# Optimization experiments

Hardware: AMD Instinct MI355X
Metric: run time of the kernel (lower is better)

The kernel has to match this reference:

```python
import jax, jax.numpy as jnp
import numpy as np
import math

N, S, D, BF, K, NT, NL = 4096, 64, 256, 24, 8, 64, 4096

def setup_inputs() -> dict:
    key = jax.random.key(0)
    ks = jax.random.split(key, 20)
    inp = {
        "values": jax.random.normal(ks[0], (N, S), dtype=jnp.float32),
        "kinds": jax.random.randint(ks[1], (N, S), 0, K, dtype=jnp.int32),
        "mask": jax.random.randint(ks[2], (N, S), 0, 2, dtype=jnp.int32),
        "prim_type": jax.random.randint(ks[3], (N,), 0, NT, dtype=jnp.int32),
        "layer_id": jax.random.randint(ks[4], (N,), 0, NL, dtype=jnp.int32),
        "meta": jax.random.normal(ks[5], (N, 4), dtype=jnp.float32),
        # frozen Fourier projection (sigma=8)
        "B_ff": jax.random.normal(ks[6], (1, BF), dtype=jnp.float32) * 8.0,
        # embeddings (N(0,1) like nn.Embedding default)
        "kind_emb_w": jax.random.normal(ks[7], (K, D), dtype=jnp.float32),
        "type_emb_w": jax.random.normal(ks[8], (NT, D), dtype=jnp.float32),
        "layer_emb_w": jax.random.normal(ks[9], (NL, D), dtype=jnp.float32),
        # per-kind MLPs: 2B -> D -> D
        "mlp_w1": jax.random.normal(ks[10], (K, 2 * BF, D), dtype=jnp.float32) / np.sqrt(2 * BF),
        "mlp_b1": jnp.zeros((K, D), dtype=jnp.float32),
        "mlp_w2": jax.random.normal(ks[11], (K, D, D), dtype=jnp.float32) / np.sqrt(D),
        "mlp_b2": jnp.zeros((K, D), dtype=jnp.float32),
        # fuse: 3D -> D -> D
        "fuse_w1": jax.random.normal(ks[12], (3 * D, D), dtype=jnp.float32) / np.sqrt(3 * D),
        "fuse_b1": jnp.zeros((D,), dtype=jnp.float32),
        "fuse_w2": jax.random.normal(ks[13], (D, D), dtype=jnp.float32) / np.sqrt(D),
        "fuse_b2": jnp.zeros((D,), dtype=jnp.float32),
        # meta_lin: 4 -> D
        "meta_w": jax.random.normal(ks[14], (4, D), dtype=jnp.float32) / 2.0,
        "meta_b": jnp.zeros((D,), dtype=jnp.float32),
    }
    return inp

def _gelu(x):
    return jax.nn.gelu(x, approximate=False)  # torch nn.GELU default = exact erf

def reference(values, kinds, mask, prim_type, layer_id, meta, B_ff,
              kind_emb_w, type_emb_w, layer_emb_w,
              mlp_w1, mlp_b1, mlp_w2, mlp_b2,
              fuse_w1, fuse_b1, fuse_w2, fuse_b2, meta_w, meta_b):
    n, s = values.shape
    d = kind_emb_w.shape[1]
    k_kinds = kind_emb_w.shape[0]
    # Fourier features over all N*S scalar slots -> [NS, 2B]
    y = (2.0 * math.pi) * values.reshape(-1, 1) @ B_ff
    ff = jnp.concatenate([jnp.sin(y), jnp.cos(y)], axis=-1)
    kf = kinds.reshape(-1)
    # kind-routed per-kind MLP (dispatch/combine expressed as masked combine)
    out = jnp.zeros((n * s, d), dtype=values.dtype)
    for k in range(k_kinds):
        h = _gelu(ff @ mlp_w1[k] + mlp_b1[k]) @ mlp_w2[k] + mlp_b2[k]
        out = jnp.where((kf == k)[:, None], h, out)
    h_slots = out.reshape(n, s, d) + kind_emb_w[kinds]
    m = mask.astype(values.dtype)
    h_slots = h_slots * m[..., None]
    denom = jnp.clip(m.sum(axis=1, keepdims=True), 1.0)  # [N,1]
    h_num = h_slots.sum(axis=1) / denom  # masked mean pooling -> [N,D]
    h = jnp.concatenate([h_num, type_emb_w[prim_type], layer_emb_w[layer_id]], axis=-1)
    fused = _gelu(h @ fuse_w1 + fuse_b1) @ fuse_w2 + fuse_b2
    return fused + meta @ meta_w + meta_b
```

## Files before the change

kernel.cpp:

```cpp
#include <hip/hip_runtime.h>
#include <math.h>


#define WIN   256
#define ROWS  4
#define NWIN  1024

#define W2F_HI   0
#define W2F_LO   524288
#define W1F_HI   1048576
#define W1F_LO   1179648
#define FW1F_HI  1310720
#define FW1F_LO  1507328
#define FW2F_HI  1703936
#define FW2F_LO  1769472
#define POOL_BYTE 3670016ull
#define CNT_BYTE  37224448ull
#define DEN_BYTE  37355520ull

typedef __attribute__((ext_vector_type(8))) short frag;
typedef __attribute__((ext_vector_type(4))) float f32x4;

__device__ __forceinline__ unsigned short f2bf_rn(float x) {
    unsigned int u = __float_as_uint(x);
    unsigned int r = (u + 0x7fffu + ((u >> 16) & 1u)) >> 16;
    return (unsigned short)r;
}
__device__ __forceinline__ float bf2f(unsigned short h) {
    return __uint_as_float(((unsigned int)h) << 16);
}
__device__ __forceinline__ void split_bf(float x, unsigned short& h, unsigned short& l) {
    unsigned short hh = f2bf_rn(x);
    h = hh;
    l = f2bf_rn(x - bf2f(hh));
}

__device__ __forceinline__ float gelu_fast(float x) {
    float u = fabsf(x) * 0.7071067811865476f;
    float t = __builtin_amdgcn_rcpf(fmaf(0.3275911f, u, 1.0f));
    float p = fmaf(fmaf(fmaf(fmaf(1.061405429f, t, -1.453152027f), t,
                             1.421413741f), t, -0.284496736f), t, 0.254829592f) * t;
    float e = __expf(-u * u);
    float er = fmaf(-p, e, 1.0f);
    er = copysignf(er, x);
    return 0.5f * x * (1.0f + er);
}

__global__ __launch_bounds__(512) void prep_kernel(
    const float* __restrict__ w1, const float* __restrict__ w2,
    const float* __restrict__ fw1, const float* __restrict__ fw2,
    short* __restrict__ ws)
{
    int tid = blockIdx.x * 512 + threadIdx.x;
    int fid = tid >> 6, ln = tid & 63;
    if (fid >= 1792) return;
    int lr = ln & 15, kq = ln >> 4;
    float v[8];
    int dhi, dlo, dsto;
    if (fid < 1024) {
        int k = fid >> 7, kst = (fid >> 4) & 7, nt = fid & 15;
        int col = nt * 16 + lr;
        #pragma unroll
        for (int b = 0; b < 8; ++b) {
            int kg = kst * 32 + kq * 8 + b;
            v[b] = w2[(k * 256 + kg) * 256 + col];
        }
        dsto = fid * 512 + ln * 8; dhi = W2F_HI; dlo = W2F_LO;
    } else if (fid < 1280) {
        int f = fid - 1024;
        int k = f >> 5, kst = (f >> 4) & 1, nt = f & 15;
        int col = nt * 16 + lr;
        #pragma unroll
        for (int b = 0; b < 8; ++b) {
            int kg = kst * 32 + kq * 8 + b;
            v[b] = (kg < 48) ? w1[(k * 48 + kg) * 256 + col] : 0.0f;
        }
        dsto = f * 512 + ln * 8; dhi = W1F_HI; dlo = W1F_LO;
    } else if (fid < 1664) {
        int f = fid - 1280;
        int kst = f >> 4, nt = f & 15;
        int col = nt * 16 + lr;
        #pragma unroll
        for (int b = 0; b < 8; ++b) {
            int kg = kst * 32 + kq * 8 + b;
            v[b] = fw1[kg * 256 + col];
        }
        dsto = f * 512 + ln * 8; dhi = FW1F_HI; dlo = FW1F_LO;
    } else {
        int f = fid - 1664;
        int kst = f >> 4, nt = f & 15;
        int col = nt * 16 + lr;
        #pragma unroll
        for (int b = 0; b < 8; ++b) {
            int kg = kst * 32 + kq * 8 + b;
            v[b] = fw2[kg * 256 + col];
        }
        dsto = f * 512 + ln * 8; dhi = FW2F_HI; dlo = FW2F_LO;
    }
    union { unsigned short u[8]; frag f; } hu, lu;
    #pragma unroll
    for (int b = 0; b < 8; ++b) split_bf(v[b], hu.u[b], lu.u[b]);
    *(frag*)(ws + dhi + dsto) = hu.f;
    *(frag*)(ws + dlo + dsto) = lu.f;
}

__global__ __launch_bounds__(512, 4) void window_kernel(
    const float* __restrict__ values, const int* __restrict__ kinds,
    const int* __restrict__ mask, const float* __restrict__ B_ff,
    const float* __restrict__ b1, const short* __restrict__ wsf,
    float* __restrict__ poolf, float* __restrict__ cntf,
    float* __restrict__ denf)
{
    __shared__ float vals[WIN];
    __shared__ unsigned char knd[WIN], msk[WIN];
    __shared__ unsigned short list[WIN + 128];
    __shared__ short chunk_kind[32];
    __shared__ short chunk_base[32];
    __shared__ int nchT_s;
    __shared__ float Bs[24];
    __shared__ float pool_s[32 * 257];
    __shared__ __align__(16) short Asl[8][2][1024];

    const short* w1f_hi = wsf + W1F_HI;
    const short* w1f_lo = wsf + W1F_LO;

    const int t = threadIdx.x, w = blockIdx.x, base = w * WIN;
    const int wv = t >> 6, ln = t & 63, lr16 = ln & 15, kq = ln >> 4;

    for (int i = t; i < WIN; i += 512) {
        vals[i] = values[base + i];
        knd[i]  = (unsigned char)kinds[base + i];
        msk[i]  = (unsigned char)mask[base + i];
    }
    if (t < 24) Bs[t] = B_ff[t];
    __syncthreads();

    if (t < 64) {
        int cnts[8];
        #pragma unroll
        for (int k = 0; k < 8; ++k) cnts[k] = 0;
        for (int c = 0; c < WIN / 64; ++c) {
            int p = c * 64 + t;
            int kd = knd[p], mk = msk[p];
            #pragma unroll
            for (int k = 0; k < 8; ++k) {
                unsigned long long bal = __ballot(mk && (kd == k));
                cnts[k] += __popcll(bal);
            }
        }
        int offk[8], run = 0;
        #pragma unroll
        for (int k = 0; k < 8; ++k) { offk[k] = run; run += (cnts[k] + 15) & ~15; }
        int fillk[8];
        #pragma unroll
        for (int k = 0; k < 8; ++k) fillk[k] = 0;
        const unsigned long long below = (1ull << t) - 1ull;
        for (int c = 0; c < WIN / 64; ++c) {
            int p = c * 64 + t;
            int kd = knd[p], mk = msk[p];
            #pragma unroll
            for (int k = 0; k < 8; ++k) {
                unsigned long long bal = __ballot(mk && (kd == k));
                if (mk && (kd == k)) {
                    int rank = __popcll(bal & below);
                    list[offk[k] + fillk[k] + rank] = (unsigned short)p;
                }
                fillk[k] += __popcll(bal);
            }
        }
        #pragma unroll
        for (int k = 0; k < 8; ++k) {
            int padded = (cnts[k] + 15) & ~15;
            for (int i = cnts[k] + t; i < padded; i += 64) list[offk[k] + i] = 0xFFFFu;
        }
        if (t == 0) {
            int ci = 0;
            #pragma unroll
            for (int k = 0; k < 8; ++k) {
                int nk = (cnts[k] + 15) >> 4;
                for (int j = 0; j < nk; ++j) {
                    chunk_kind[ci] = (short)k;
                    chunk_base[ci] = (short)(offk[k] + j * 16);
                    ++ci;
                }
            }
            nchT_s = ci;
        }
    } else if (t < 96) {
        int i = t - 64, r = i >> 3, k = i & 7, c = 0;
        for (int s = 0; s < 64; ++s) c += (msk[r * 64 + s] && knd[r * 64 + s] == k) ? 1 : 0;
        cntf[(w * ROWS + r) * 8 + k] = (float)c;
    } else if (t < 100) {
        int r = t - 96, c = 0;
        for (int s = 0; s < 64; ++s) c += msk[r * 64 + s];
        denf[w * ROWS + r] = 1.0f / (float)(c > 0 ? c : 1);
    } else if (t >= 128) {
        for (int i = t - 128; i < 32 * 257; i += 384) pool_s[i] = 0.0f;
    }
    __syncthreads();

    const int nchT = nchT_s;

    for (int ci = wv; ci < nchT; ci += 8) {
        const int k = (int)chunk_kind[ci];
        const int cb = (int)chunk_base[ci];

        #pragma unroll
        for (int half = 0; half < 2; ++half) {
            int tt = ln + half * 64;
            int s = tt >> 3, g = tt & 7;
            union { unsigned short u[8]; frag f; } hu, lu;
            if (g < 6) {
                int e = list[cb + s];
                float v = vals[e & (WIN - 1)];
                int iscos = (g >= 3);
                int j0 = (iscos ? (g - 3) : g) * 8;
                #pragma unroll
                for (int b = 0; b < 8; ++b) {
                    float rev = __builtin_amdgcn_fractf(v * Bs[j0 + b]);
                    float sv = iscos ? __builtin_amdgcn_cosf(rev)
                                     : __builtin_amdgcn_sinf(rev);
                    split_bf(sv, hu.u[b], lu.u[b]);
                }
            } else {
                #pragma unroll
                for (int b = 0; b < 8; ++b) { hu.u[b] = 0; lu.u[b] = 0; }
            }
            int ao = s * 64 + ((g ^ (s & 7)) << 3);
            *(frag*)&Asl[wv][0][ao] = hu.f;
            *(frag*)&Asl[wv][1][ao] = lu.f;
        }
        frag ah[2], al[2];
        #pragma unroll
        for (int kst = 0; kst < 2; ++kst) {
            int gi = kst * 4 + kq;
            int ao = lr16 * 64 + ((gi ^ (lr16 & 7)) << 3);
            ah[kst] = *(const frag*)&Asl[wv][0][ao];
            al[kst] = *(const frag*)&Asl[wv][1][ao];
        }
        for (int ntg = 0; ntg < 4; ++ntg) {
            f32x4 acc[4];
            #pragma unroll
            for (int q = 0; q < 4; ++q) acc[q] = (f32x4)0.0f;
            #pragma unroll
            for (int q = 0; q < 4; ++q) {
                int nt = ntg * 4 + q;
                size_t bo0 = (((size_t)k * 2 + 0) * 16 + nt) * 512 + ln * 8;
                size_t bo1 = (((size_t)k * 2 + 1) * 16 + nt) * 512 + ln * 8;
                frag bh0 = *(const frag*)(w1f_hi + bo0);
                frag bl0 = *(const frag*)(w1f_lo + bo0);
                frag bh1 = *(const frag*)(w1f_hi + bo1);
                frag bl1 = *(const frag*)(w1f_lo + bo1);
                acc[q] = __builtin_amdgcn_mfma_f32_16x16x32_bf16(ah[0], bh0, acc[q], 0, 0, 0);
                acc[q] = __builtin_amdgcn_mfma_f32_16x16x32_bf16(al[0], bh0, acc[q], 0, 0, 0);
                acc[q] = __builtin_amdgcn_mfma_f32_16x16x32_bf16(ah[0], bl0, acc[q], 0, 0, 0);
                acc[q] = __builtin_amdgcn_mfma_f32_16x16x32_bf16(ah[1], bh1, acc[q], 0, 0, 0);
                acc[q] = __builtin_amdgcn_mfma_f32_16x16x32_bf16(al[1], bh1, acc[q], 0, 0, 0);
                acc[q] = __builtin_amdgcn_mfma_f32_16x16x32_bf16(ah[1], bl1, acc[q], 0, 0, 0);
            }
            #pragma unroll
            for (int q = 0; q < 4; ++q) {
                int nt = ntg * 4 + q;
                int col = nt * 16 + lr16;
                float b1v = b1[k * 256 + col];
                #pragma unroll
                for (int r = 0; r < 4; ++r) {
                    int s = kq * 4 + r;
                    int e = list[cb + s];
                    if (e != 0xFFFF) {
                        float g = gelu_fast(acc[q][r] + b1v);
                        atomicAdd(&pool_s[((e >> 6) * 8 + k) * 257 + col], g);
                    }
                }
            }
        }
    }
    __syncthreads();

    for (int i = t; i < 32 * 256; i += 512) {
        int rk = i >> 8, c = i & 255;
        int r = rk >> 3, k = rk & 7;
        poolf[((size_t)k * 4096 + w * ROWS + r) * 256 + c] = pool_s[rk * 257 + c];
    }
}

__global__ __launch_bounds__(512) void fuse_kernel(
    const short* __restrict__ ws, const float* __restrict__ poolf,
    const float* __restrict__ cntf, const float* __restrict__ denf,
    const int* __restrict__ pt, const int* __restrict__ lid,
    const float* __restrict__ meta, const float* __restrict__ type_emb,
    const float* __restrict__ layer_emb, const float* __restrict__ b2,
    const float* __restrict__ kind_emb, const float* __restrict__ fb1,
    const float* __restrict__ fb2, const float* __restrict__ meta_w,
    const float* __restrict__ meta_b, float* __restrict__ out)
{
    __shared__ __align__(16) short Af[2][2][4096];
    __shared__ __align__(16) float hz[4096];
    __shared__ float cnt_s[128], den_s[16], meta_s[64];
    __shared__ int pt_s[16], lid_s[16];

    const short* w2f_hi  = ws + W2F_HI;
    const short* w2f_lo  = ws + W2F_LO;
    const short* fw1f_hi = ws + FW1F_HI;
    const short* fw1f_lo = ws + FW1F_LO;
    const short* fw2f_hi = ws + FW2F_HI;
    const short* fw2f_lo = ws + FW2F_LO;

    const int t = threadIdx.x, blk = blockIdx.x, rb = blk * 16;
    const int wv = t >> 6, ln = t & 63, lr16 = ln & 15, kq = ln >> 4;

    if (t < 16) { pt_s[t] = pt[rb + t]; lid_s[t] = lid[rb + t]; den_s[t] = denf[rb + t]; }
    else if (t < 144) cnt_s[t - 16] = cntf[rb * 8 + (t - 16)];
    else if (t < 208) meta_s[t - 144] = meta[rb * 4 + (t - 144)];

    const int sr = t >> 5, sg = t & 31;
    const int skst = sg >> 2, skq = sg & 3;
    const int slane = skq * 16 + sr;
    const int sdst = slane * 64 + ((skst ^ (sr & 7)) << 3);

    auto stage = [&](int k, int buf) {
        const float* src = poolf + ((size_t)k * 4096 + rb + sr) * 256 + sg * 8;
        f32x4 u0 = *(const f32x4*)src;
        f32x4 u1 = *(const f32x4*)(src + 4);
        union { unsigned short u[8]; frag f; } hu, lu;
        #pragma unroll
        for (int b = 0; b < 4; ++b) {
            split_bf(u0[b], hu.u[b], lu.u[b]);
            split_bf(u1[b], hu.u[b + 4], lu.u[b + 4]);
        }
        *(frag*)&Af[buf][0][sdst] = hu.f;
        *(frag*)&Af[buf][1][sdst] = lu.f;
    };

    stage(0, 0);
    __syncthreads();

    f32x4 acc[2];
    acc[0] = (f32x4)0.0f; acc[1] = (f32x4)0.0f;

    for (int k = 0; k < 8; ++k) {
        const int buf = k & 1;
        if (k < 7) stage(k + 1, buf ^ 1);
        #pragma unroll 2
        for (int kst = 0; kst < 8; ++kst) {
            int ao = ln * 64 + ((kst ^ (ln & 7)) << 3);
            frag ah = *(const frag*)&Af[buf][0][ao];
            frag al = *(const frag*)&Af[buf][1][ao];
            #pragma unroll
            for (int n = 0; n < 2; ++n) {
                size_t bo = (((size_t)k * 8 + kst) * 16 + (wv * 2 + n)) * 512 + ln * 8;
                frag bh = *(const frag*)(w2f_hi + bo);
                frag bl = *(const frag*)(w2f_lo + bo);
                acc[n] = __builtin_amdgcn_mfma_f32_16x16x32_bf16(ah, bh, acc[n], 0, 0, 0);
                acc[n] = __builtin_amdgcn_mfma_f32_16x16x32_bf16(al, bh, acc[n], 0, 0, 0);
                acc[n] = __builtin_amdgcn_mfma_f32_16x16x32_bf16(ah, bl, acc[n], 0, 0, 0);
            }
        }
        __syncthreads();
    }

    #pragma unroll
    for (int n = 0; n < 2; ++n) {
        int col = (wv * 2 + n) * 16 + lr16;
        float bks[8];
        #pragma unroll
        for (int k = 0; k < 8; ++k) bks[k] = b2[k * 256 + col] + kind_emb[k * 256 + col];
        #pragma unroll
        for (int r = 0; r < 4; ++r) {
            int row = kq * 4 + r;
            float hv = acc[n][r];
            #pragma unroll
            for (int k = 0; k < 8; ++k) hv = fmaf(cnt_s[row * 8 + k], bks[k], hv);
            hv *= den_s[row];
            hz[row * 256 + ((((col >> 2) ^ (row & 7)) << 2) | (col & 3))] = hv;
        }
    }
    __syncthreads();

    f32x4 az[2];
    az[0] = (f32x4)0.0f; az[1] = (f32x4)0.0f;

    for (int kst = 0; kst < 24; ++kst) {
        const int row = lr16;
        union { unsigned short u[8]; frag f; } hu, lu;
        if (kst < 8) {
            int c0 = kst * 8 + kq * 2;
            f32x4 u0 = *(const f32x4*)&hz[row * 256 + ((c0 ^ (row & 7)) << 2)];
            f32x4 u1 = *(const f32x4*)&hz[row * 256 + (((c0 + 1) ^ (row & 7)) << 2)];
            #pragma unroll
            for (int b = 0; b < 4; ++b) {
                split_bf(u0[b], hu.u[b], lu.u[b]);
                split_bf(u1[b], hu.u[b + 4], lu.u[b + 4]);
            }
        } else {
            const float* eb = (kst < 16) ? type_emb : layer_emb;
            const int* ids = (kst < 16) ? pt_s : lid_s;
            int ko = (kst & 7) * 32 + kq * 8;
            const float* sp = eb + (size_t)ids[row] * 256 + ko;
            f32x4 u0 = *(const f32x4*)sp;
            f32x4 u1 = *(const f32x4*)(sp + 4);
            #pragma unroll
            for (int b = 0; b < 4; ++b) {
                split_bf(u0[b], hu.u[b], lu.u[b]);
                split_bf(u1[b], hu.u[b + 4], lu.u[b + 4]);
            }
        }
        frag ah = hu.f, al = lu.f;
        #pragma unroll
        for (int n = 0; n < 2; ++n) {
            size_t bo = ((size_t)kst * 16 + (wv * 2 + n)) * 512 + ln * 8;
            frag bh = *(const frag*)(fw1f_hi + bo);
            frag bl = *(const frag*)(fw1f_lo + bo);
            az[n] = __builtin_amdgcn_mfma_f32_16x16x32_bf16(ah, bh, az[n], 0, 0, 0);
            az[n] = __builtin_amdgcn_mfma_f32_16x16x32_bf16(al, bh, az[n], 0, 0, 0);
            az[n] = __builtin_amdgcn_mfma_f32_16x16x32_bf16(ah, bl, az[n], 0, 0, 0);
        }
    }
    __syncthreads();

    #pragma unroll
    for (int n = 0; n < 2; ++n) {
        int col = (wv * 2 + n) * 16 + lr16;
        float fb1v = fb1[col];
        #pragma unroll
        for (int r = 0; r < 4; ++r) {
            int row = kq * 4 + r;
            float z = gelu_fast(az[n][r] + fb1v);
            hz[row * 256 + ((((col >> 2) ^ (row & 7)) << 2) | (col & 3))] = z;
        }
    }
    __syncthreads();

    f32x4 ao[2];
    ao[0] = (f32x4)0.0f; ao[1] = (f32x4)0.0f;

    for (int kst = 0; kst < 8; ++kst) {
        const int row = lr16;
        int c0 = kst * 8 + kq * 2;
        f32x4 u0 = *(const f32x4*)&hz[row * 256 + ((c0 ^ (row & 7)) << 2)];
        f32x4 u1 = *(const f32x4*)&hz[row * 256 + (((c0 + 1) ^ (row & 7)) << 2)];
        union { unsigned short u[8]; frag f; } hu, lu;
        #pragma unroll
        for (int b = 0; b < 4; ++b) {
            split_bf(u0[b], hu.u[b], lu.u[b]);
            split_bf(u1[b], hu.u[b + 4], lu.u[b + 4]);
        }
        frag ah = hu.f, al = lu.f;
        #pragma unroll
        for (int n = 0; n < 2; ++n) {
            size_t bo = ((size_t)kst * 16 + (wv * 2 + n)) * 512 + ln * 8;
            frag bh = *(const frag*)(fw2f_hi + bo);
            frag bl = *(const frag*)(fw2f_lo + bo);
            ao[n] = __builtin_amdgcn_mfma_f32_16x16x32_bf16(ah, bh, ao[n], 0, 0, 0);
            ao[n] = __builtin_amdgcn_mfma_f32_16x16x32_bf16(al, bh, ao[n], 0, 0, 0);
            ao[n] = __builtin_amdgcn_mfma_f32_16x16x32_bf16(ah, bl, ao[n], 0, 0, 0);
        }
    }

    #pragma unroll
    for (int n = 0; n < 2; ++n) {
        int col = (wv * 2 + n) * 16 + lr16;
        float ob = fb2[col] + meta_b[col];
        float mw0 = meta_w[col], mw1 = meta_w[256 + col];
        float mw2 = meta_w[512 + col], mw3 = meta_w[768 + col];
        #pragma unroll
        for (int r = 0; r < 4; ++r) {
            int row = kq * 4 + r;
            float o = ao[n][r] + ob;
            o = fmaf(meta_s[row * 4 + 0], mw0, o);
            o = fmaf(meta_s[row * 4 + 1], mw1, o);
            o = fmaf(meta_s[row * 4 + 2], mw2, o);
            o = fmaf(meta_s[row * 4 + 3], mw3, o);
            out[(size_t)(rb + row) * 256 + col] = o;
        }
    }
}

extern "C" void kernel_launch(void* const* d_in, const int* in_sizes, int n_in,
                              void* d_out, int out_size, void* d_ws, size_t ws_size,
                              hipStream_t stream) {
    const float* values    = (const float*)d_in[0];
    const int*   kinds     = (const int*)d_in[1];
    const int*   mask      = (const int*)d_in[2];
    const int*   prim_type = (const int*)d_in[3];
    const int*   layer_id  = (const int*)d_in[4];
    const float* meta      = (const float*)d_in[5];
    const float* B_ff      = (const float*)d_in[6];
    const float* kind_emb  = (const float*)d_in[7];
    const float* type_emb  = (const float*)d_in[8];
    const float* layer_emb = (const float*)d_in[9];
    const float* mlp_w1    = (const float*)d_in[10];
    const float* mlp_b1    = (const float*)d_in[11];
    const float* mlp_w2    = (const float*)d_in[12];
    const float* mlp_b2    = (const float*)d_in[13];
    const float* fuse_w1   = (const float*)d_in[14];
    const float* fuse_b1   = (const float*)d_in[15];
    const float* fuse_w2   = (const float*)d_in[16];
    const float* fuse_b2   = (const float*)d_in[17];
    const float* meta_w    = (const float*)d_in[18];
    const float* meta_b    = (const float*)d_in[19];

    short* ws    = (short*)d_ws;
    float* poolf = (float*)((char*)d_ws + POOL_BYTE);
    float* cntf  = (float*)((char*)d_ws + CNT_BYTE);
    float* denf  = (float*)((char*)d_ws + DEN_BYTE);
    float* out   = (float*)d_out;

    prep_kernel<<<224, 512, 0, stream>>>(mlp_w1, mlp_w2, fuse_w1, fuse_w2, ws);
    window_kernel<<<NWIN, 512, 0, stream>>>(values, kinds, mask, B_ff, mlp_b1,
                                            ws, poolf, cntf, denf);
    fuse_kernel<<<256, 512, 0, stream>>>(ws, poolf, cntf, denf, prim_type, layer_id,
                                         meta, type_emb, layer_emb, mlp_b2, kind_emb,
                                         fuse_b1, fuse_b2, meta_w, meta_b, out);
}
```

Before: 268.7 us.

## Split window kernel into scan, fill, and per-kind MLP kernels with LDS weights

```diff
diff --git a/kernel.cpp b/kernel.cpp
--- a/kernel.cpp
+++ b/kernel.cpp
@@ -1,10 +1,6 @@
 #include <hip/hip_runtime.h>
 #include <math.h>
 
-
-#define WIN   256
-#define ROWS  4
-#define NWIN  1024
 
 #define W2F_HI   0
 #define W2F_LO   524288
@@ -17,6 +13,8 @@
 #define POOL_BYTE 3670016ull
 #define CNT_BYTE  37224448ull
 #define DEN_BYTE  37355520ull
+#define LIST_BYTE 37371904ull
+#define QCNT_BYTE 38420480ull
 
 typedef __attribute__((ext_vector_type(8))) short frag;
 typedef __attribute__((ext_vector_type(4))) float f32x4;
@@ -104,183 +102,187 @@
     *(frag*)(ws + dlo + dsto) = lu.f;
 }
 
-__global__ __launch_bounds__(512, 4) void window_kernel(
-    const float* __restrict__ values, const int* __restrict__ kinds,
-    const int* __restrict__ mask, const float* __restrict__ B_ff,
-    const float* __restrict__ b1, const short* __restrict__ wsf,
-    float* __restrict__ poolf, float* __restrict__ cntf,
-    float* __restrict__ denf)
+__global__ __launch_bounds__(256) void scan_count(
+    const int* __restrict__ kinds, const int* __restrict__ mask,
+    float* __restrict__ cntf, float* __restrict__ denf,
+    int* __restrict__ qcnt)
 {
-    __shared__ float vals[WIN];
-    __shared__ unsigned char knd[WIN], msk[WIN];
-    __shared__ unsigned short list[WIN + 128];
-    __shared__ short chunk_kind[32];
-    __shared__ short chunk_base[32];
-    __shared__ int nchT_s;
+    __shared__ int qc[8];
+    const int t = threadIdx.x, b = blockIdx.x;
+    const int wv = t >> 6, ln = t & 63;
+    if (t < 8) qc[t] = 0;
+    __syncthreads();
+
+    for (int j = 0; j < 4; ++j) {
+        int R = b * 16 + wv * 4 + j;
+        int kd = kinds[R * 64 + ln];
+        int mk = mask[R * 64 + ln];
+        unsigned long long mb = __ballot(mk != 0);
+        int tot = __popcll(mb);
+        int myc = 0;
+        #pragma unroll
+        for (int k = 0; k < 8; ++k) {
+            unsigned long long bal = __ballot(mk && (kd == k));
+            int c = __popcll(bal);
+            myc = (ln == k) ? c : myc;
+        }
+        if (ln < 8) {
+            cntf[R * 8 + ln] = (float)myc;
+            atomicAdd(&qc[ln], myc);
+        }
+        if (ln == 0) denf[R] = 1.0f / (float)(tot > 0 ? tot : 1);
+    }
+    __syncthreads();
+    if (t < 8) qcnt[b * 8 + t] = qc[t];
+}
+
+__global__ __launch_bounds__(256) void scan_fill(
+    const int* __restrict__ kinds, const int* __restrict__ mask,
+    const int* __restrict__ qcnt, unsigned short* __restrict__ listb)
+{
+    const int t = threadIdx.x, b = blockIdx.x;
+    const int w = b >> 2, q = b & 3;
+    const int wv = t >> 6, ln = t & 63;
+    const unsigned long long below = (1ull << ln) - 1ull;
+
+    for (int half = 0; half < 2; ++half) {
+        const int k = wv * 2 + half;
+        int base = 0;
+        for (int qq = 0; qq < q; ++qq) base += qcnt[(w * 4 + qq) * 8 + k];
+        int fill = 0;
+        unsigned short* lp = listb + (w * 8 + k) * 1024;
+        for (int c = 0; c < 16; ++c) {
+            int p = q * 1024 + c * 64 + ln;
+            int kd = kinds[w * 4096 + p];
+            int mk = mask[w * 4096 + p];
+            unsigned long long bal = __ballot(mk && (kd == k));
+            if (mk && (kd == k)) {
+                int rank = __popcll(bal & below);
+                int idx = base + fill + rank;
+                if (idx < 1024) lp[idx] = (unsigned short)p;
+            }
+            fill += __popcll(bal);
+        }
+        if (q == 3) {
+            int len = base + fill;
+            int lp64 = (len + 63) & ~63;
+            for (int i = len + ln; i < lp64 && i < 1024; i += 64) lp[i] = 0xFFFFu;
+        }
+    }
+}
+
+__global__ __launch_bounds__(512) void mlp_kernel(
+    const float* __restrict__ values, const short* __restrict__ wsf,
+    const unsigned short* __restrict__ listb, const int* __restrict__ qcnt,
+    const float* __restrict__ B_ff, const float* __restrict__ b1,
+    float* __restrict__ poolf)
+{
+    __shared__ __align__(16) short Bhi[16384], Blo[16384];
+    __shared__ __align__(16) short At[2][4096];
+    __shared__ float pool[64 * 257];
+    __shared__ unsigned short e_tile[64];
     __shared__ float Bs[24];
-    __shared__ float pool_s[32 * 257];
-    __shared__ __align__(16) short Asl[8][2][1024];
-
-    const short* w1f_hi = wsf + W1F_HI;
-    const short* w1f_lo = wsf + W1F_LO;
-
-    const int t = threadIdx.x, w = blockIdx.x, base = w * WIN;
+
+    const int t = threadIdx.x, blk = blockIdx.x;
+    const int w = blk >> 3, k = blk & 7;
     const int wv = t >> 6, ln = t & 63, lr16 = ln & 15, kq = ln >> 4;
-
-    for (int i = t; i < WIN; i += 512) {
-        vals[i] = values[base + i];
-        knd[i]  = (unsigned char)kinds[base + i];
-        msk[i]  = (unsigned char)mask[base + i];
+    const int mt = wv >> 1, nh = wv & 1;
+
+    {
+        const uint4* gh = (const uint4*)(wsf + W1F_HI + k * 16384);
+        const uint4* gl = (const uint4*)(wsf + W1F_LO + k * 16384);
+        uint4* sh = (uint4*)Bhi;
+        uint4* sl = (uint4*)Blo;
+        #pragma unroll
+        for (int i = 0; i < 4; ++i) {
+            sh[t + i * 512] = gh[t + i * 512];
+            sl[t + i * 512] = gl[t + i * 512];
+        }
     }
     if (t < 24) Bs[t] = B_ff[t];
-    __syncthreads();
-
-    if (t < 64) {
-        int cnts[8];
-        #pragma unroll
-        for (int k = 0; k < 8; ++k) cnts[k] = 0;
-        for (int c = 0; c < WIN / 64; ++c) {
-            int p = c * 64 + t;
-            int kd = knd[p], mk = msk[p];
-            #pragma unroll
-            for (int k = 0; k < 8; ++k) {
-                unsigned long long bal = __ballot(mk && (kd == k));
-                cnts[k] += __popcll(bal);
-            }
-        }
-        int offk[8], run = 0;
-        #pragma unroll
-        for (int k = 0; k < 8; ++k) { offk[k] = run; run += (cnts[k] + 15) & ~15; }
-        int fillk[8];
-        #pragma unroll
-        for (int k = 0; k < 8; ++k) fillk[k] = 0;
-        const unsigned long long below = (1ull << t) - 1ull;
-        for (int c = 0; c < WIN / 64; ++c) {
-            int p = c * 64 + t;
-            int kd = knd[p], mk = msk[p];
-            #pragma unroll
-            for (int k = 0; k < 8; ++k) {
-                unsigned long long bal = __ballot(mk && (kd == k));
-                if (mk && (kd == k)) {
-                    int rank = __popcll(bal & below);
-                    list[offk[k] + fillk[k] + rank] = (unsigned short)p;
-                }
-                fillk[k] += __popcll(bal);
-            }
-        }
-        #pragma unroll
-        for (int k = 0; k < 8; ++k) {
-            int padded = (cnts[k] + 15) & ~15;
-            for (int i = cnts[k] + t; i < padded; i += 64) list[offk[k] + i] = 0xFFFFu;
-        }
-        if (t == 0) {
-            int ci = 0;
-            #pragma unroll
-            for (int k = 0; k < 8; ++k) {
-                int nk = (cnts[k] + 15) >> 4;
-                for (int j = 0; j < nk; ++j) {
-                    chunk_kind[ci] = (short)k;
-                    chunk_base[ci] = (short)(offk[k] + j * 16);
-                    ++ci;
-                }
-            }
-            nchT_s = ci;
-        }
-    } else if (t < 96) {
-        int i = t - 64, r = i >> 3, k = i & 7, c = 0;
-        for (int s = 0; s < 64; ++s) c += (msk[r * 64 + s] && knd[r * 64 + s] == k) ? 1 : 0;
-        cntf[(w * ROWS + r) * 8 + k] = (float)c;
-    } else if (t < 100) {
-        int r = t - 96, c = 0;
-        for (int s = 0; s < 64; ++s) c += msk[r * 64 + s];
-        denf[w * ROWS + r] = 1.0f / (float)(c > 0 ? c : 1);
-    } else if (t >= 128) {
-        for (int i = t - 128; i < 32 * 257; i += 384) pool_s[i] = 0.0f;
-    }
-    __syncthreads();
-
-    const int nchT = nchT_s;
-
-    for (int ci = wv; ci < nchT; ci += 8) {
-        const int k = (int)chunk_kind[ci];
-        const int cb = (int)chunk_base[ci];
-
-        #pragma unroll
-        for (int half = 0; half < 2; ++half) {
-            int tt = ln + half * 64;
-            int s = tt >> 3, g = tt & 7;
+    for (int i = t; i < 64 * 257; i += 512) pool[i] = 0.0f;
+
+    int len = 0;
+    #pragma unroll
+    for (int qq = 0; qq < 4; ++qq) len += qcnt[(w * 4 + qq) * 8 + k];
+    const int ntl = (len + 63) >> 6;
+
+    float b1r[8];
+    #pragma unroll
+    for (int n = 0; n < 8; ++n) b1r[n] = b1[k * 256 + (nh * 8 + n) * 16 + lr16];
+
+    __syncthreads();
+
+    for (int m = 0; m < ntl; ++m) {
+        {
+            int s = t >> 3, g = t & 7;
+            unsigned short e = listb[(w * 8 + k) * 1024 + m * 64 + s];
+            if (g == 0) e_tile[s] = e;
             union { unsigned short u[8]; frag f; } hu, lu;
-            if (g < 6) {
-                int e = list[cb + s];
-                float v = vals[e & (WIN - 1)];
+            if (g < 6 && e != 0xFFFFu) {
+                float v = values[w * 4096 + e];
                 int iscos = (g >= 3);
                 int j0 = (iscos ? (g - 3) : g) * 8;
                 #pragma unroll
-                for (int b = 0; b < 8; ++b) {
-                    float rev = __builtin_amdgcn_fractf(v * Bs[j0 + b]);
+                for (int bb = 0; bb < 8; ++bb) {
+                    float rev = __builtin_amdgcn_fractf(v * Bs[j0 + bb]);
                     float sv = iscos ? __builtin_amdgcn_cosf(rev)
                                      : __builtin_amdgcn_sinf(rev);
-                    split_bf(sv, hu.u[b], lu.u[b]);
+                    split_bf(sv, hu.u[bb], lu.u[bb]);
                 }
             } else {
                 #pragma unroll
-                for (int b = 0; b < 8; ++b) { hu.u[b] = 0; lu.u[b] = 0; }
+                for (int bb = 0; bb < 8; ++bb) { hu.u[bb] = 0; lu.u[bb] = 0; }
             }
             int ao = s * 64 + ((g ^ (s & 7)) << 3);
-            *(frag*)&Asl[wv][0][ao] = hu.f;
-            *(frag*)&Asl[wv][1][ao] = lu.f;
-        }
+            *(frag*)&At[0][ao] = hu.f;
+            *(frag*)&At[1][ao] = lu.f;
+        }
+        __syncthreads();
+
         frag ah[2], al[2];
         #pragma unroll
         for (int kst = 0; kst < 2; ++kst) {
             int gi = kst * 4 + kq;
-            int ao = lr16 * 64 + ((gi ^ (lr16 & 7)) << 3);
-            ah[kst] = *(const frag*)&Asl[wv][0][ao];
-            al[kst] = *(const frag*)&Asl[wv][1][ao];
-        }
-        for (int ntg = 0; ntg < 4; ++ntg) {
-            f32x4 acc[4];
+            int ao = (mt * 16 + lr16) * 64 + ((gi ^ (lr16 & 7)) << 3);
+            ah[kst] = *(const frag*)&At[0][ao];
+            al[kst] = *(const frag*)&At[1][ao];
+        }
+        unsigned short e4[4];
+        #pragma unroll
+        for (int r = 0; r < 4; ++r) e4[r] = e_tile[mt * 16 + kq * 4 + r];
+
+        #pragma unroll
+        for (int n = 0; n < 8; ++n) {
+            int nt = nh * 8 + n;
+            int o0 = (0 * 16 + nt) * 512 + ln * 8;
+            int o1 = (1 * 16 + nt) * 512 + ln * 8;
+            frag bh0 = *(const frag*)(Bhi + o0);
+            frag bl0 = *(const frag*)(Blo + o0);
+            frag bh1 = *(const frag*)(Bhi + o1);
+            frag bl1 = *(const frag*)(Blo + o1);
+            f32x4 acc = (f32x4)0.0f;
+            acc = __builtin_amdgcn_mfma_f32_16x16x32_bf16(ah[0], bh0, acc, 0, 0, 0);
+            acc = __builtin_amdgcn_mfma_f32_16x16x32_bf16(al[0], bh0, acc, 0, 0, 0);
+            acc = __builtin_amdgcn_mfma_f32_16x16x32_bf16(ah[0], bl0, acc, 0, 0, 0);
+            acc = __builtin_amdgcn_mfma_f32_16x16x32_bf16(ah[1], bh1, acc, 0, 0, 0);
+            acc = __builtin_amdgcn_mfma_f32_16x16x32_bf16(al[1], bh1, acc, 0, 0, 0);
+            acc = __builtin_amdgcn_mfma_f32_16x16x32_bf16(ah[1], bl1, acc, 0, 0, 0);
             #pragma unroll
-            for (int q = 0; q < 4; ++q) acc[q] = (f32x4)0.0f;
-            #pragma unroll
-            for (int q = 0; q < 4; ++q) {
-                int nt = ntg * 4 + q;
-                size_t bo0 = (((size_t)k * 2 + 0) * 16 + nt) * 512 + ln * 8;
-                size_t bo1 = (((size_t)k * 2 + 1) * 16 + nt) * 512 + ln * 8;
-                frag bh0 = *(const frag*)(w1f_hi + bo0);
-                frag bl0 = *(const frag*)(w1f_lo + bo0);
-                frag bh1 = *(const frag*)(w1f_hi + bo1);
-                frag bl1 = *(const frag*)(w1f_lo + bo1);
-                acc[q] = __builtin_amdgcn_mfma_f32_16x16x32_bf16(ah[0], bh0, acc[q], 0, 0, 0);
-                acc[q] = __builtin_amdgcn_mfma_f32_16x16x32_bf16(al[0], bh0, acc[q], 0, 0, 0);
-                acc[q] = __builtin_amdgcn_mfma_f32_16x16x32_bf16(ah[0], bl0, acc[q], 0, 0, 0);
-                acc[q] = __builtin_amdgcn_mfma_f32_16x16x32_bf16(ah[1], bh1, acc[q], 0, 0, 0);
-                acc[q] = __builtin_amdgcn_mfma_f32_16x16x32_bf16(al[1], bh1, acc[q], 0, 0, 0);
-                acc[q] = __builtin_amdgcn_mfma_f32_16x16x32_bf16(ah[1], bl1, acc[q], 0, 0, 0);
-            }
-            #pragma unroll
-            for (int q = 0; q < 4; ++q) {
-                int nt = ntg * 4 + q;
-                int col = nt * 16 + lr16;
-                float b1v = b1[k * 256 + col];
-                #pragma unroll
-                for (int r = 0; r < 4; ++r) {
-                    int s = kq * 4 + r;
-                    int e = list[cb + s];
-                    if (e != 0xFFFF) {
-                        float g = gelu_fast(acc[q][r] + b1v);
-                        atomicAdd(&pool_s[((e >> 6) * 8 + k) * 257 + col], g);
-                    }
+            for (int r = 0; r < 4; ++r) {
+                unsigned short e = e4[r];
+                if (e != 0xFFFFu) {
+                    float g = gelu_fast(acc[r] + b1r[n]);
+                    atomicAdd(&pool[(e >> 6) * 257 + nt * 16 + lr16], g);
                 }
             }
         }
-    }
-    __syncthreads();
-
-    for (int i = t; i < 32 * 256; i += 512) {
-        int rk = i >> 8, c = i & 255;
-        int r = rk >> 3, k = rk & 7;
-        poolf[((size_t)k * 4096 + w * ROWS + r) * 256 + c] = pool_s[rk * 257 + c];
+        __syncthreads();
+    }
+
+    for (int i = t; i < 64 * 256; i += 512) {
+        int r = i >> 8, c = i & 255;
+        poolf[((size_t)k * 4096 + w * 64 + r) * 256 + c] = pool[r * 257 + c];
     }
 }
 
@@ -431,8 +433,8 @@
     }
     __syncthreads();
 
-    f32x4 ao[2];
-    ao[0] = (f32x4)0.0f; ao[1] = (f32x4)0.0f;
+    f32x4 ao2[2];
+    ao2[0] = (f32x4)0.0f; ao2[1] = (f32x4)0.0f;
 
     for (int kst = 0; kst < 8; ++kst) {
         const int row = lr16;
@@ -451,9 +453,9 @@
             size_t bo = ((size_t)kst * 16 + (wv * 2 + n)) * 512 + ln * 8;
             frag bh = *(const frag*)(fw2f_hi + bo);
             frag bl = *(const frag*)(fw2f_lo + bo);
-            ao[n] = __builtin_amdgcn_mfma_f32_16x16x32_bf16(ah, bh, ao[n], 0, 0, 0);
-            ao[n] = __builtin_amdgcn_mfma_f32_16x16x32_bf16(al, bh, ao[n], 0, 0, 0);
-            ao[n] = __builtin_amdgcn_mfma_f32_16x16x32_bf16(ah, bl, ao[n], 0, 0, 0);
+            ao2[n] = __builtin_amdgcn_mfma_f32_16x16x32_bf16(ah, bh, ao2[n], 0, 0, 0);
+            ao2[n] = __builtin_amdgcn_mfma_f32_16x16x32_bf16(al, bh, ao2[n], 0, 0, 0);
+            ao2[n] = __builtin_amdgcn_mfma_f32_16x16x32_bf16(ah, bl, ao2[n], 0, 0, 0);
         }
     }
 
@@ -466,7 +468,7 @@
         #pragma unroll
         for (int r = 0; r < 4; ++r) {
             int row = kq * 4 + r;
-            float o = ao[n][r] + ob;
+            float o = ao2[n][r] + ob;
             o = fmaf(meta_s[row * 4 + 0], mw0, o);
             o = fmaf(meta_s[row * 4 + 1], mw1, o);
             o = fmaf(meta_s[row * 4 + 2], mw2, o);
@@ -500,15 +502,18 @@
     const float* meta_w    = (const float*)d_in[18];
     const float* meta_b    = (const float*)d_in[19];
 
-    short* ws    = (short*)d_ws;
-    float* poolf = (float*)((char*)d_ws + POOL_BYTE);
-    float* cntf  = (float*)((char*)d_ws + CNT_BYTE);
-    float* denf  = (float*)((char*)d_ws + DEN_BYTE);
-    float* out   = (float*)d_out;
+    short*          ws    = (short*)d_ws;
+    float*          poolf = (float*)((char*)d_ws + POOL_BYTE);
+    float*          cntf  = (float*)((char*)d_ws + CNT_BYTE);
+    float*          denf  = (float*)((char*)d_ws + DEN_BYTE);
+    unsigned short* listb = (unsigned short*)((char*)d_ws + LIST_BYTE);
+    int*            qcnt  = (int*)((char*)d_ws + QCNT_BYTE);
+    float*          out   = (float*)d_out;
 
     prep_kernel<<<224, 512, 0, stream>>>(mlp_w1, mlp_w2, fuse_w1, fuse_w2, ws);
-    window_kernel<<<NWIN, 512, 0, stream>>>(values, kinds, mask, B_ff, mlp_b1,
-                                            ws, poolf, cntf, denf);
+    scan_count<<<256, 256, 0, stream>>>(kinds, mask, cntf, denf, qcnt);
+    scan_fill<<<256, 256, 0, stream>>>(kinds, mask, qcnt, listb);
+    mlp_kernel<<<512, 512, 0, stream>>>(values, ws, listb, qcnt, B_ff, mlp_b1, poolf);
     fuse_kernel<<<256, 512, 0, stream>>>(ws, poolf, cntf, denf, prim_type, layer_id,
                                          meta, type_emb, layer_emb, mlp_b2, kind_emb,
                                          fuse_b1, fuse_b2, meta_w, meta_b, out);
```

After: 284.0 us. +5.7%, slower.
